# Performance work log

Measured on AMD Instinct MI355X. Metric: run time of the kernel, lower is better.

## Reference

```python
import jax, jax.numpy as jnp
import numpy as np

GAMMA = 2.0
ALPHA_CLASS = 0.01
ALPHA_COORD = 1.0

def _xywh_to_xyxy(b):
    # [.., 4] (x, y, w, h) -> (x1, y1, x2, y2)
    return jnp.concatenate([b[..., :2], b[..., :2] + b[..., 2:]], axis=-1)

def _jaccard(a, b):
    # a: [A,4] xyxy, b: [N,4] xyxy -> IoU [A,N]
    lt = jnp.maximum(a[:, None, :2], b[None, :, :2])
    rb = jnp.minimum(a[:, None, 2:], b[None, :, 2:])
    wh = jnp.clip(rb - lt, 0.0)
    inter = wh[..., 0] * wh[..., 1]
    area_a = (a[:, 2] - a[:, 0]) * (a[:, 3] - a[:, 1])
    area_b = (b[:, 2] - b[:, 0]) * (b[:, 3] - b[:, 1])
    return inter / (area_a[:, None] + area_b[None, :] - inter)

def _match_mask(thr, anchors, gt_xywh, num_obj):
    # Returns positive (anchor, gt) pair mask [A, N_max], honoring gt[:num_obj].
    A = anchors.shape[0]
    N = gt_xywh.shape[0]
    gt_boxes = _xywh_to_xyxy(gt_xywh)
    ious = _jaccard(anchors, gt_boxes)              # [A, N]
    valid = jnp.arange(N) < num_obj                 # [N]
    ious_v = jnp.where(valid[None, :], ious, -jnp.inf)
    best_gt_idx = jnp.argmax(ious_v, axis=0)        # [N] best anchor per gt
    forced = jnp.arange(A)[:, None] == best_gt_idx[None, :]  # positive_mask[best,i]=1
    return ((ious > thr) | forced) & valid[None, :]

def _class_loss_item(thr, classes, anchors, gt, num_obj):
    # classes: [A,2] probs (col0 = background, col1 = face)
    mask = _match_mask(thr, anchors, gt, num_obj)   # [A, N]
    counts = jnp.sum(mask, axis=1)                  # [A] multiplicity of each anchor in positive_idx
    is_pos = counts > 0                             # dedup, as index_fill_ does
    probs = jnp.where(is_pos, classes[:, 1], classes[:, 0])
    focal = -((1.0 - probs) ** GAMMA) * jnp.log(probs)
    # extra = focal_loss.index_select(0, positive_idx) keeps duplicates -> weight by counts
    extra = jnp.sum(counts.astype(focal.dtype) * focal)
    return jnp.sum(focal) + 10.0 * extra

def setup_inputs() -> dict:
    key = jax.random.key(0)
    B, A, N = 16, 131072, 64
    k1, k2, k3, k4, k5, k6 = jax.random.split(key, 6)
    # anchors in xyxy, valid boxes in [0,1]
    a_xy = jax.random.uniform(k1, (A, 2), jnp.float32, 0.0, 0.8)
    a_wh = jax.random.uniform(k2, (A, 2), jnp.float32, 0.05, 0.2)
    anchors = jnp.concatenate([a_xy, a_xy + a_wh], axis=-1)
    # class probabilities strictly in (0,1) for log()
    batch_classes = jax.random.uniform(k3, (B, A, 2), jnp.float32, 0.05, 0.95)
    g_xy = jax.random.uniform(k4, (B, N, 2), jnp.float32, 0.0, 0.8)
    g_wh = jax.random.uniform(k5, (B, N, 2), jnp.float32, 0.05, 0.2)
    batch_gt = jnp.concatenate([g_xy, g_wh], axis=-1)  # xywh
    batch_num_objects = jax.random.randint(k6, (B,), 1, N + 1, jnp.int32)
    return {
        "threshhold": jnp.float32(0.5),
        "batch_classes": batch_classes,
        "anchors": anchors,
        "batch_gt": batch_gt,
        "batch_num_objects": batch_num_objects,
    }

def reference(threshhold, batch_classes, anchors, batch_gt, batch_num_objects):
    R = batch_classes.shape[0]
    per_item = jax.vmap(lambda c, g, n: _class_loss_item(threshhold, c, anchors, g, n))
    class_loss = jnp.sum(per_item(batch_classes, batch_gt, batch_num_objects))
    class_loss = class_loss * ALPHA_CLASS / R
    # Faithful to the source: coord_loss is initialized to zero and never accumulated
    coord_loss = jnp.zeros((), batch_classes.dtype) * ALPHA_COORD / R
    total_loss = class_loss + coord_loss
    return (total_loss, class_loss, coord_loss)
```

## Files before the change

### kernel.cpp

```cpp
#include <hip/hip_runtime.h>

typedef unsigned long long ull;

#define NANCH    131072
#define NMAX     64
#define NBATCH   16
#define THREADS  256
#define APT      4
#define ACH      (THREADS*APT)
#define NPAIR    8
#define NB_CNT   ((NANCH/ACH)*NPAIR)
#define AC_ANCH  256
#define NCHUNK_A (NANCH/AC_ANCH)
#define BPB_A    (NCHUNK_A/4)
#define MAXB     16
#define NB_ARG   (MAXB*BPB_A)
#define GRID_MAIN (NB_CNT+NB_ARG)


__global__ __launch_bounds__(64) void k_setup(
    const int* __restrict__ nobj, ull* __restrict__ cells,
    int* __restrict__ pairs, int* __restrict__ lanepk, int* __restrict__ nbund)
{
    int tid = threadIdx.x;
    for (int i = tid; i < NBATCH*NMAX; i += 64) cells[i] = 0ull;
    for (int i = tid; i < MAXB*NMAX; i += 64) lanepk[i] = -1;
    __syncthreads();
    if (tid) return;
    int ord[NBATCH], key[NBATCH];
    for (int i = 0; i < NBATCH; ++i) { ord[i] = i; key[i] = nobj[i]; }
    for (int i = 1; i < NBATCH; ++i) {
        int k = key[i], o = ord[i], j = i-1;
        while (j >= 0 && key[j] < k) { key[j+1]=key[j]; ord[j+1]=ord[j]; --j; }
        key[j+1] = k; ord[j+1] = o;
    }
    for (int p = 0; p < NPAIR; ++p) {
        pairs[2*p]   = ord[p];
        pairs[2*p+1] = ord[NBATCH-1-p];
    }
    int rem[MAXB];
    int nb = 0;
    for (int i = 0; i < NBATCH; ++i) {
        int n = key[i], f = -1;
        for (int x = 0; x < nb; ++x) if (rem[x] >= n) { f = x; break; }
        if (f < 0) { f = nb++; rem[f] = NMAX; }
        int st = NMAX - rem[f];
        for (int k = 0; k < n; ++k) lanepk[f*NMAX + st + k] = (ord[i] << 8) | k;
        rem[f] -= n;
    }
    *nbund = nb;
}

__global__ __launch_bounds__(THREADS, 6) void k_main(
    const float* __restrict__ thr_p,
    const float* __restrict__ classes,
    const float* __restrict__ anchors,
    const float* __restrict__ gt,
    const int*   __restrict__ nobj,
    const int*   __restrict__ pairs,
    const int*   __restrict__ lanepk,
    const int*   __restrict__ nbund,
    ull* __restrict__ cells,
    double* __restrict__ partials)
{
    int bid = blockIdx.x;
    int tid = threadIdx.x;
    float thr = *thr_p;
    float q   = thr / (1.0f + thr);

    if (bid < NB_CNT) {
        int chunk = bid >> 3, pr = bid & 7;
        int b0 = pairs[2*pr], b1 = pairs[2*pr+1];
        int no0 = nobj[b0], no1 = nobj[b1];

        __shared__ float4 sbox[2*NMAX];
        __shared__ float  sqg[2*NMAX];
        __shared__ double sw[4];
        if (tid < 2*NMAX) {
            int s = tid >> 6, n = tid & 63;
            int b  = s ? b1 : b0;
            int no = s ? no1 : no0;
            float4 g = reinterpret_cast<const float4*>(gt)[b*NMAX + n];
            float x2 = g.x + g.z, y2 = g.y + g.w;
            float4 box = make_float4(g.x, g.y, x2, y2);
            float  qg  = q * ((x2 - g.x) * (y2 - g.y));
            if (n >= no) { box = make_float4(4.f,4.f,4.f,4.f); qg = __builtin_inff(); }
            sbox[tid] = box; sqg[tid] = qg;
        }
        __syncthreads();

        float ax1[APT], ay1[APT], ax2[APT], ay2[APT], qa[APT];
        int abase = chunk * ACH + tid;
        #pragma unroll
        for (int k = 0; k < APT; ++k) {
            float4 v = reinterpret_cast<const float4*>(anchors)[abase + k*THREADS];
            ax1[k]=v.x; ay1[k]=v.y; ax2[k]=v.z; ay2[k]=v.w;
            qa[k] = q * ((v.z - v.x) * (v.w - v.y));
        }

        int wv = tid >> 6, ln = tid & 63;
        double acc = 0.0;
        #pragma unroll
        for (int s = 0; s < 2; ++s) {
            int b    = s ? b1 : b0;
            int no   = s ? no1 : no0;
            int no4  = (no + 3) & ~3;
            int base = s * NMAX;
            int cnt[APT];
            #pragma unroll
            for (int k = 0; k < APT; ++k) cnt[k] = 0;

            for (int n = 0; n < no4; n += 4) {
                #pragma unroll
                for (int u = 0; u < 4; ++u) {
                    float4 g  = sbox[base + n + u];
                    float  qg = sqg[base + n + u];
                    #pragma unroll
                    for (int k = 0; k < APT; ++k) {
                        float lx = fmaxf(ax1[k], g.x);
                        float ly = fmaxf(ay1[k], g.y);
                        float rx = fminf(ax2[k], g.z);
                        float ry = fminf(ay2[k], g.w);
                        float w  = fmaxf(rx - lx, 0.f);
                        float h  = fmaxf(ry - ly, 0.f);
                        float inter = w * h;
                        cnt[k] += (inter > qa[k] + qg) ? 1 : 0;
                    }
                }
            }
            const float2* cp = reinterpret_cast<const float2*>(classes) + (size_t)b * NANCH;
            #pragma unroll
            for (int k = 0; k < APT; ++k) {
                float2 c = cp[abase + k*THREADS];
                float p  = (cnt[k] > 0) ? c.y : c.x;
                float om = 1.0f - p;
                float f  = -om * om * __logf(p);
                acc += (double)(f * (1.0f + 10.0f * (float)cnt[k]));
            }
        }
        #pragma unroll
        for (int off = 32; off; off >>= 1) acc += __shfl_xor(acc, off, 64);
        if (ln == 0) sw[wv] = acc;
        __syncthreads();
        if (tid == 0) partials[bid] = sw[0] + sw[1] + sw[2] + sw[3];

    } else {
        int r    = bid - NB_CNT;
        int bu   = r >> 7;
        int blkc = r & (BPB_A - 1);
        if (bu >= *nbund) return;
        int wv = tid >> 6, ln = tid & 63;
        int abase = (blkc*4 + wv) * AC_ANCH;

        int lp = lanepk[bu*NMAX + ln];
        bool valid = lp >= 0;
        int gidx = valid ? ((lp >> 8)*NMAX + (lp & 255)) : 0;
        float4 gg = reinterpret_cast<const float4*>(gt)[gidx];
        float gx2 = gg.x + gg.z, gy2 = gg.y + gg.w;
        float gar = (gx2 - gg.x) * (gy2 - gg.y);

        float bn[4] = {-1.f,-1.f,-1.f,-1.f};
        float bs[4] = { 1.f, 1.f, 1.f, 1.f};
        int   bj[4] = {0,0,0,0};
        const float4* ap = reinterpret_cast<const float4*>(anchors) + abase;
        for (int j = 0; j < AC_ANCH; j += 4) {
            #pragma unroll
            for (int u = 0; u < 4; ++u) {
                float4 v = ap[j + u];
                float aar = (v.z - v.x) * (v.w - v.y);
                float lx = fmaxf(v.x, gg.x);
                float ly = fmaxf(v.y, gg.y);
                float rx = fminf(v.z, gx2);
                float ry = fminf(v.w, gy2);
                float w  = fmaxf(rx - lx, 0.f);
                float h  = fmaxf(ry - ly, 0.f);
                float inter = w * h;
                float sa    = aar + gar;
                bool better = inter * bs[u] > bn[u] * sa;
                bn[u] = better ? inter : bn[u];
                bs[u] = better ? sa    : bs[u];
                bj[u] = better ? (j+u) : bj[u];
            }
        }
        if (valid) {
            ull best = 0;
            #pragma unroll
            for (int u = 0; u < 4; ++u) {
                float rr = bn[u] * __builtin_amdgcn_rcpf(bs[u]);
                unsigned aidx = (unsigned)(abase + bj[u]);
                ull pk = ((ull)__float_as_uint(rr) << 32)
                       | (ull)(0x7FFFFFFFu - aidx);
                best = pk > best ? pk : best;
            }
            atomicMax(&cells[(lp >> 8)*NMAX + (lp & 255)], best);
        }
    }
}

__global__ __launch_bounds__(1024) void k_tail(
    const float* __restrict__ thr_p,
    const float* __restrict__ classes,
    const float* __restrict__ anchors,
    const float* __restrict__ gt,
    const int*   __restrict__ nobj,
    const ull*   __restrict__ cells,
    const double* __restrict__ partials,
    float* __restrict__ out)
{
    int tid = threadIdx.x;
    int b = tid >> 6, n = tid & 63;
    float thr = *thr_p;
    float q   = thr / (1.0f + thr);

    __shared__ float4 sbox[NBATCH*NMAX];
    __shared__ float  sqg[NBATCH*NMAX];
    __shared__ int    sidx[NBATCH*NMAX];
    __shared__ double sdelta[NBATCH];
    __shared__ double sw[16];

    int n_obj = nobj[b];
    {
        float4 g = reinterpret_cast<const float4*>(gt)[b*NMAX + n];
        float x2 = g.x + g.z, y2 = g.y + g.w;
        sbox[tid] = make_float4(g.x, g.y, x2, y2);
        float gar = (x2 - g.x) * (y2 - g.y);
        sqg[tid]  = q * gar;
    }
    __syncthreads();

    int bi = -1; bool need = false;
    float4 av = make_float4(0.f,0.f,0.f,0.f);
    float qa = 0.f;
    if (n < n_obj) {
        ull pkv = cells[tid];
        bi = (int)(0x7FFFFFFFu - (unsigned)(pkv & 0xFFFFFFFFull));
        av = reinterpret_cast<const float4*>(anchors)[bi];
        float aar = (av.z - av.x) * (av.w - av.y);
        qa = q * aar;
        float4 g = sbox[tid];
        float lx = fmaxf(av.x, g.x), ly = fmaxf(av.y, g.y);
        float rx = fminf(av.z, g.z), ry = fminf(av.w, g.w);
        float w  = fmaxf(rx - lx, 0.f), h = fmaxf(ry - ly, 0.f);
        float inter = w * h;
        need = !(inter > qa + sqg[tid]);
    }
    sidx[tid] = need ? bi : -1;
    __syncthreads();

    double delta = 0.0;
    if (need) {
        bool first = true; int extra = 0;
        int base = b * NMAX;
        for (int m = 0; m < NMAX; ++m) {
            if (sidx[base + m] == bi) { if (m < n) first = false; ++extra; }
        }
        if (first) {
            int count = 0;
            for (int m = 0; m < n_obj; ++m) {
                float4 g = sbox[base + m];
                float lx = fmaxf(av.x, g.x), ly = fmaxf(av.y, g.y);
                float rx = fminf(av.z, g.z), ry = fminf(av.w, g.w);
                float w  = fmaxf(rx - lx, 0.f), h = fmaxf(ry - ly, 0.f);
                float inter = w * h;
                count += (inter > qa + sqg[base + m]) ? 1 : 0;
            }
            float2 c = reinterpret_cast<const float2*>(classes)[(size_t)b * NANCH + bi];
            float po = (count > 0) ? c.y : c.x;
            float oo = 1.0f - po;
            float fo = -oo * oo * __logf(po);
            float oldc = fo * (1.0f + 10.0f * (float)count);
            int cn = count + extra;
            float pn = (cn > 0) ? c.y : c.x;
            float on = 1.0f - pn;
            float fn = -on * on * __logf(pn);
            float newc = fn * (1.0f + 10.0f * (float)cn);
            delta = (double)newc - (double)oldc;
        }
    }
    #pragma unroll
    for (int off = 32; off; off >>= 1) delta += __shfl_xor(delta, off, 64);
    if (n == 0) sdelta[b] = delta;
    __syncthreads();

    double v = partials[tid];
    if (tid < NBATCH) v += sdelta[tid];
    #pragma unroll
    for (int off = 32; off; off >>= 1) v += __shfl_xor(v, off, 64);
    if ((tid & 63) == 0) sw[tid >> 6] = v;
    __syncthreads();
    if (tid == 0) {
        double tot = 0.0;
        #pragma unroll
        for (int i = 0; i < 16; ++i) tot += sw[i];
        double cls = tot * (0.01 / 16.0);
        out[0] = (float)cls;
        out[1] = (float)cls;
        out[2] = 0.0f;
    }
}

extern "C" void kernel_launch(void* const* d_in, const int* in_sizes, int n_in,
                              void* d_out, int out_size, void* d_ws, size_t ws_size,
                              hipStream_t stream) {
    const float* thr     = (const float*)d_in[0];
    const float* classes = (const float*)d_in[1];
    const float* anchors = (const float*)d_in[2];
    const float* gt      = (const float*)d_in[3];
    const int*   nobj    = (const int*)d_in[4];
    float* out = (float*)d_out;

    char* ws = (char*)d_ws;
    ull*    cells    = (ull*)(ws + 0);
    int*    pairs    = (int*)(ws + 8192);
    int*    lanepk   = (int*)(ws + 8256);
    int*    nbund    = (int*)(ws + 12352);
    double* partials = (double*)(ws + 12416);

    k_setup<<<1, 64, 0, stream>>>(nobj, cells, pairs, lanepk, nbund);
    k_main<<<GRID_MAIN, THREADS, 0, stream>>>(thr, classes, anchors, gt, nobj,
                                              pairs, lanepk, nbund, cells, partials);
    k_tail<<<1, 1024, 0, stream>>>(thr, classes, anchors, gt, nobj, cells, partials, out);
}
```

Before: 106.9 us.

## Precompute anchor areas, interleave count/argmax blocks, widen argmax unroll to 8

The setup kernel now precomputes the area of each anchor into the workspace when it is large enough, and the argmax path reads those areas instead of recomputing them. The argmax inner loop is unrolled 8-wide with 8 independent best-so-far accumulators and loads all eight anchors before computing. Count blocks and argmax blocks are interleaved 1:2 across the grid so the two work types run side by side instead of in two phases. The occupancy hint on k_main is dropped. The extra accumulators raise register pressure, and the setup kernel does an additional pass over the anchors.

```diff
diff --git a/kernel.cpp b/kernel.cpp
--- a/kernel.cpp
+++ b/kernel.cpp
@@ -11,20 +11,31 @@
 #define NPAIR    8
 #define NB_CNT   ((NANCH/ACH)*NPAIR)
 #define AC_ANCH  256
-#define NCHUNK_A (NANCH/AC_ANCH)
-#define BPB_A    (NCHUNK_A/4)
+#define BPB_A    128
 #define MAXB     16
 #define NB_ARG   (MAXB*BPB_A)
 #define GRID_MAIN (NB_CNT+NB_ARG)
 
-
-__global__ __launch_bounds__(64) void k_setup(
-    const int* __restrict__ nobj, ull* __restrict__ cells,
-    int* __restrict__ pairs, int* __restrict__ lanepk, int* __restrict__ nbund)
+#define WS_PAREA_OFF 24576
+#define WS_NEED (WS_PAREA_OFF + NANCH*4)
+
+template<bool BIG>
+__global__ __launch_bounds__(256) void k_setup(
+    const int* __restrict__ nobj, const float* __restrict__ anchors,
+    ull* __restrict__ cells, int* __restrict__ pairs,
+    int* __restrict__ lanepk, int* __restrict__ nbund,
+    float* __restrict__ parea)
 {
     int tid = threadIdx.x;
-    for (int i = tid; i < NBATCH*NMAX; i += 64) cells[i] = 0ull;
-    for (int i = tid; i < MAXB*NMAX; i += 64) lanepk[i] = -1;
+    if (BIG) {
+        for (int i = blockIdx.x*256 + tid; i < NANCH; i += gridDim.x*256) {
+            float4 v = reinterpret_cast<const float4*>(anchors)[i];
+            parea[i] = (v.z - v.x) * (v.w - v.y);
+        }
+    }
+    if (blockIdx.x != 0) return;
+    for (int i = tid; i < NBATCH*NMAX; i += 256) cells[i] = 0ull;
+    for (int i = tid; i < MAXB*NMAX; i += 256) lanepk[i] = -1;
     __syncthreads();
     if (tid) return;
     int ord[NBATCH], key[NBATCH];
@@ -51,7 +62,8 @@
     *nbund = nb;
 }
 
-__global__ __launch_bounds__(THREADS, 6) void k_main(
+template<bool BIG>
+__global__ __launch_bounds__(THREADS) void k_main(
     const float* __restrict__ thr_p,
     const float* __restrict__ classes,
     const float* __restrict__ anchors,
@@ -60,15 +72,18 @@
     const int*   __restrict__ pairs,
     const int*   __restrict__ lanepk,
     const int*   __restrict__ nbund,
+    const float* __restrict__ parea,
     ull* __restrict__ cells,
     double* __restrict__ partials)
 {
-    int bid = blockIdx.x;
-    int tid = threadIdx.x;
+    int bid0 = blockIdx.x;
+    int tid  = threadIdx.x;
     float thr = *thr_p;
     float q   = thr / (1.0f + thr);
-
-    if (bid < NB_CNT) {
+    bool is_cnt = (bid0 % 3) == 0;
+    int  bid    = is_cnt ? (bid0 / 3) : ((bid0 / 3) * 2 + (bid0 % 3) - 1);
+
+    if (is_cnt) {
         int chunk = bid >> 3, pr = bid & 7;
         int b0 = pairs[2*pr], b1 = pairs[2*pr+1];
         int no0 = nobj[b0], no1 = nobj[b1];
@@ -145,9 +160,8 @@
         if (tid == 0) partials[bid] = sw[0] + sw[1] + sw[2] + sw[3];
 
     } else {
-        int r    = bid - NB_CNT;
-        int bu   = r >> 7;
-        int blkc = r & (BPB_A - 1);
+        int bu   = bid >> 7;
+        int blkc = bid & (BPB_A - 1);
         if (bu >= *nbund) return;
         int wv = tid >> 6, ln = tid & 63;
         int abase = (blkc*4 + wv) * AC_ANCH;
@@ -159,23 +173,34 @@
         float gx2 = gg.x + gg.z, gy2 = gg.y + gg.w;
         float gar = (gx2 - gg.x) * (gy2 - gg.y);
 
-        float bn[4] = {-1.f,-1.f,-1.f,-1.f};
-        float bs[4] = { 1.f, 1.f, 1.f, 1.f};
-        int   bj[4] = {0,0,0,0};
-        const float4* ap = reinterpret_cast<const float4*>(anchors) + abase;
-        for (int j = 0; j < AC_ANCH; j += 4) {
-            #pragma unroll
-            for (int u = 0; u < 4; ++u) {
-                float4 v = ap[j + u];
-                float aar = (v.z - v.x) * (v.w - v.y);
-                float lx = fmaxf(v.x, gg.x);
-                float ly = fmaxf(v.y, gg.y);
-                float rx = fminf(v.z, gx2);
-                float ry = fminf(v.w, gy2);
+        float bn[8], bs[8]; int bj[8];
+        #pragma unroll
+        for (int u = 0; u < 8; ++u) { bn[u] = -1.f; bs[u] = 1.f; bj[u] = 0; }
+        const float4* ap  = reinterpret_cast<const float4*>(anchors) + abase;
+        const float4* pa4 = reinterpret_cast<const float4*>(parea + abase);
+        for (int j = 0; j < AC_ANCH; j += 8) {
+            float4 v[8]; float ar[8];
+            #pragma unroll
+            for (int u = 0; u < 8; ++u) v[u] = ap[j + u];
+            if (BIG) {
+                float4 a0 = pa4[(j >> 2)], a1 = pa4[(j >> 2) + 1];
+                ar[0]=a0.x; ar[1]=a0.y; ar[2]=a0.z; ar[3]=a0.w;
+                ar[4]=a1.x; ar[5]=a1.y; ar[6]=a1.z; ar[7]=a1.w;
+            } else {
+                #pragma unroll
+                for (int u = 0; u < 8; ++u)
+                    ar[u] = (v[u].z - v[u].x) * (v[u].w - v[u].y);
+            }
+            #pragma unroll
+            for (int u = 0; u < 8; ++u) {
+                float lx = fmaxf(v[u].x, gg.x);
+                float ly = fmaxf(v[u].y, gg.y);
+                float rx = fminf(v[u].z, gx2);
+                float ry = fminf(v[u].w, gy2);
                 float w  = fmaxf(rx - lx, 0.f);
                 float h  = fmaxf(ry - ly, 0.f);
                 float inter = w * h;
-                float sa    = aar + gar;
+                float sa    = ar[u] + gar;
                 bool better = inter * bs[u] > bn[u] * sa;
                 bn[u] = better ? inter : bn[u];
                 bs[u] = better ? sa    : bs[u];
@@ -185,7 +210,7 @@
         if (valid) {
             ull best = 0;
             #pragma unroll
-            for (int u = 0; u < 4; ++u) {
+            for (int u = 0; u < 8; ++u) {
                 float rr = bn[u] * __builtin_amdgcn_rcpf(bs[u]);
                 unsigned aidx = (unsigned)(abase + bj[u]);
                 ull pk = ((ull)__float_as_uint(rr) << 32)
@@ -315,9 +340,19 @@
     int*    lanepk   = (int*)(ws + 8256);
     int*    nbund    = (int*)(ws + 12352);
     double* partials = (double*)(ws + 12416);
-
-    k_setup<<<1, 64, 0, stream>>>(nobj, cells, pairs, lanepk, nbund);
-    k_main<<<GRID_MAIN, THREADS, 0, stream>>>(thr, classes, anchors, gt, nobj,
-                                              pairs, lanepk, nbund, cells, partials);
+    float*  parea    = (float*)(ws + WS_PAREA_OFF);
+
+    bool big = ws_size >= (size_t)WS_NEED;
+    if (big) {
+        k_setup<true><<<128, 256, 0, stream>>>(nobj, anchors, cells, pairs,
+                                               lanepk, nbund, parea);
+        k_main<true><<<GRID_MAIN, THREADS, 0, stream>>>(thr, classes, anchors, gt,
+                nobj, pairs, lanepk, nbund, parea, cells, partials);
+    } else {
+        k_setup<false><<<1, 256, 0, stream>>>(nobj, anchors, cells, pairs,
+                                              lanepk, nbund, parea);
+        k_main<false><<<GRID_MAIN, THREADS, 0, stream>>>(thr, classes, anchors, gt,
+                nobj, pairs, lanepk, nbund, parea, cells, partials);
+    }
     k_tail<<<1, 1024, 0, stream>>>(thr, classes, anchors, gt, nobj, cells, partials, out);
 }
```

Result: faster. 99.54 us (-6.9%).

## Spatially bin anchors and cull GT boxes per wave with fused argmax

Applied to the files above, without the earlier changes.

Adds a counting-sort pass (histogram, scan, scatter) that buckets anchors into a 16x16 spatial grid. The main kernel then checks each wave's anchor bounding box against each GT box and skips GT boxes that cannot overlap. The per-GT best-anchor argmax moves into the same pass, using a wave reduction plus atomicMax, so the separate full-anchor argmax sweep goes away. Background focal loss is summed over all anchors in separate blocks, and positive anchors are corrected on top. This costs three extra small launches and a larger workspace, and the old two-pass path is kept as a fallback with interleaved blocks and a wider unroll.

```diff
diff --git a/kernel.cpp b/kernel.cpp
--- a/kernel.cpp
+++ b/kernel.cpp
@@ -2,29 +2,221 @@
 
 typedef unsigned long long ull;
 
-#define NANCH    131072
-#define NMAX     64
-#define NBATCH   16
-#define THREADS  256
+#define NANCH   131072
+#define NMAX    64
+#define NBATCH  16
+#define THREADS 256
+
+#define OFF_PART  8192
+#define OFF_CH    16384
+#define OFF_CID   278528
+#define OFF_SRT   802816
+#define OFF_SIX   2899968
+#define WS_NEED   3424256
+#define OFF_PAIRS 16384
+#define OFF_LANE  16448
+#define OFF_NB    20544
+
+__device__ __forceinline__ float focal_f(float p) {
+    float om = 1.0f - p;
+    return -om * om * __logf(p);
+}
+
+__global__ __launch_bounds__(256) void k_hist(
+    const float* __restrict__ anchors, int* __restrict__ cellid,
+    int* __restrict__ chunkH)
+{
+    __shared__ int h[256];
+    int tid = threadIdx.x, c = blockIdx.x;
+    h[tid] = 0; __syncthreads();
+    #pragma unroll
+    for (int k = 0; k < 2; ++k) {
+        int i = c*512 + tid + k*256;
+        float4 v = reinterpret_cast<const float4*>(anchors)[i];
+        int cx = (int)(v.x * 20.0f); cx = cx < 0 ? 0 : (cx > 15 ? 15 : cx);
+        int cy = (int)(v.y * 20.0f); cy = cy < 0 ? 0 : (cy > 15 ? 15 : cy);
+        int cell = cy*16 + cx;
+        cellid[i] = cell;
+        atomicAdd(&h[cell], 1);
+    }
+    __syncthreads();
+    chunkH[c*256 + tid] = h[tid];
+}
+
+__global__ __launch_bounds__(256) void k_scan(
+    int* __restrict__ CH, ull* __restrict__ cells)
+{
+    __shared__ int total[256];
+    __shared__ int cstart[256];
+    int b = threadIdx.x;
+    int run = 0;
+    for (int c = 0; c < 256; ++c) { int h = CH[c*256+b]; CH[c*256+b] = run; run += h; }
+    total[b] = run;
+    __syncthreads();
+    if (b == 0) { int cs = 0; for (int i = 0; i < 256; ++i) { cstart[i] = cs; cs += total[i]; } }
+    __syncthreads();
+    int s = cstart[b];
+    for (int c = 0; c < 256; ++c) CH[c*256+b] += s;
+    for (int i = b; i < NBATCH*NMAX; i += 256) cells[i] = 0x7FFFFFFFull;
+}
+
+__global__ __launch_bounds__(256) void k_scatter(
+    const float* __restrict__ anchors, const int* __restrict__ cellid,
+    const int* __restrict__ CB, float4* __restrict__ sorted,
+    int* __restrict__ sidx)
+{
+    __shared__ int lc[512];
+    int tid = threadIdx.x, c = blockIdx.x;
+    lc[tid]     = cellid[c*512 + tid];
+    lc[tid+256] = cellid[c*512 + 256 + tid];
+    __syncthreads();
+    int i0 = 2*tid, i1 = 2*tid + 1;
+    int c0 = lc[i0], c1 = lc[i1];
+    int r0 = 0, r1 = 0;
+    for (int j = 0; j < i0; ++j) { int cj = lc[j]; r0 += (cj==c0)?1:0; r1 += (cj==c1)?1:0; }
+    r1 += (c0 == c1) ? 1 : 0;
+    int g0 = c*512 + i0, g1 = c*512 + i1;
+    int p0 = CB[c*256 + c0] + r0, p1 = CB[c*256 + c1] + r1;
+    sorted[p0] = reinterpret_cast<const float4*>(anchors)[g0]; sidx[p0] = g0;
+    sorted[p1] = reinterpret_cast<const float4*>(anchors)[g1]; sidx[p1] = g1;
+}
+
+__global__ __launch_bounds__(THREADS) void k_main_s(
+    const float* __restrict__ thr_p,
+    const float* __restrict__ classes,
+    const float4* __restrict__ sorted,
+    const int*   __restrict__ sidx,
+    const float* __restrict__ gt,
+    const int*   __restrict__ nobj,
+    ull* __restrict__ cells,
+    double* __restrict__ partials)
+{
+    int bid = blockIdx.x, tid = threadIdx.x;
+    int wv = tid >> 6, ln = tid & 63;
+    float thr = *thr_p;
+    float q   = thr / (1.0f + thr);
+    __shared__ double sw[4];
+    double acc = 0.0;
+
+    if ((bid & 1) == 0) {
+        int aid  = bid >> 1;
+        int sblk = aid >> 2, bg = aid & 3;
+        __shared__ float4 sgt[4*64];
+        __shared__ float2 sgq[4*64];
+        __shared__ int    snobj[4];
+        {
+            int bb = tid >> 6, n = tid & 63;
+            int b = bg + 4*bb;
+            float4 g = reinterpret_cast<const float4*>(gt)[b*NMAX + n];
+            float x2 = g.x + g.z, y2 = g.y + g.w;
+            sgt[tid] = make_float4(g.x, g.y, x2, y2);
+            float gar = (x2 - g.x) * (y2 - g.y);
+            sgq[tid] = make_float2(q * gar, gar);
+            if (n == 0) snobj[bb] = nobj[b];
+        }
+        __syncthreads();
+
+        int abase = sblk*1024 + wv*256;
+        float4 A[4]; float aar[4], qa[4]; int orig[4];
+        float bx1 = 1e30f, by1 = 1e30f, bx2 = -1e30f, by2 = -1e30f;
+        #pragma unroll
+        for (int k = 0; k < 4; ++k) {
+            int s = abase + k*64 + ln;
+            A[k] = sorted[s]; orig[k] = sidx[s];
+            aar[k] = (A[k].z - A[k].x) * (A[k].w - A[k].y);
+            qa[k]  = q * aar[k];
+            bx1 = fminf(bx1, A[k].x); by1 = fminf(by1, A[k].y);
+            bx2 = fmaxf(bx2, A[k].z); by2 = fmaxf(by2, A[k].w);
+        }
+        #pragma unroll
+        for (int off = 32; off; off >>= 1) {
+            bx1 = fminf(bx1, __shfl_xor(bx1, off, 64));
+            by1 = fminf(by1, __shfl_xor(by1, off, 64));
+            bx2 = fmaxf(bx2, __shfl_xor(bx2, off, 64));
+            by2 = fmaxf(by2, __shfl_xor(by2, off, 64));
+        }
+
+        const float2* cls2 = reinterpret_cast<const float2*>(classes);
+        for (int bb = 0; bb < 4; ++bb) {
+            int b = bg + 4*bb, no = snobj[bb], base = bb*64;
+            int cnt[4] = {0,0,0,0};
+            for (int n = 0; n < no; ++n) {
+                float4 g = sgt[base + n];
+                if (!(g.x < bx2 && g.z > bx1 && g.y < by2 && g.w > by1)) continue;
+                float2 gq = sgq[base + n];
+                ull mypk = 0;
+                #pragma unroll
+                for (int k = 0; k < 4; ++k) {
+                    float lx = fmaxf(A[k].x, g.x);
+                    float ly = fmaxf(A[k].y, g.y);
+                    float rx = fminf(A[k].z, g.z);
+                    float ry = fminf(A[k].w, g.w);
+                    float w  = fmaxf(rx - lx, 0.f);
+                    float h  = fmaxf(ry - ly, 0.f);
+                    float inter = w * h;
+                    cnt[k] += (inter > qa[k] + gq.x) ? 1 : 0;
+                    float sa = aar[k] + gq.y;
+                    float r  = inter * __builtin_amdgcn_rcpf(sa);
+                    ull pk = ((ull)__float_as_uint(r) << 32)
+                           | (ull)(0x7FFFFFFFu - (unsigned)orig[k]);
+                    mypk = pk > mypk ? pk : mypk;
+                }
+                #pragma unroll
+                for (int off = 32; off; off >>= 1) {
+                    ull o = __shfl_xor(mypk, off, 64);
+                    mypk = o > mypk ? o : mypk;
+                }
+                if (ln == 0) atomicMax(&cells[b*NMAX + n], mypk);
+            }
+            int any = cnt[0] | cnt[1] | cnt[2] | cnt[3];
+            if (__ballot(any != 0)) {
+                #pragma unroll
+                for (int k = 0; k < 4; ++k) {
+                    if (cnt[k] > 0) {
+                        float2 cc = cls2[(size_t)b * NANCH + orig[k]];
+                        float fg  = focal_f(cc.y);
+                        float bgf = focal_f(cc.x);
+                        acc += (double)(fg * (1.0f + 10.0f * (float)cnt[k]))
+                             - (double)bgf;
+                    }
+                }
+            }
+        }
+    } else {
+        int rid = bid >> 1;
+        const float4* c4 = reinterpret_cast<const float4*>(classes);
+        size_t base = (size_t)rid * 2048 + tid;
+        #pragma unroll
+        for (int it = 0; it < 8; ++it) {
+            float4 v = c4[base + (size_t)it * 256];
+            acc += (double)focal_f(v.x) + (double)focal_f(v.z);
+        }
+    }
+
+    #pragma unroll
+    for (int off = 32; off; off >>= 1) acc += __shfl_xor(acc, off, 64);
+    if (ln == 0) sw[wv] = acc;
+    __syncthreads();
+    if (tid == 0) partials[bid] = sw[0] + sw[1] + sw[2] + sw[3];
+}
+
 #define APT      4
 #define ACH      (THREADS*APT)
 #define NPAIR    8
 #define NB_CNT   ((NANCH/ACH)*NPAIR)
 #define AC_ANCH  256
-#define NCHUNK_A (NANCH/AC_ANCH)
-#define BPB_A    (NCHUNK_A/4)
+#define BPB_A    128
 #define MAXB     16
 #define NB_ARG   (MAXB*BPB_A)
-#define GRID_MAIN (NB_CNT+NB_ARG)
-
-
-__global__ __launch_bounds__(64) void k_setup(
+#define GRID_FB  (NB_CNT+NB_ARG)
+
+__global__ __launch_bounds__(256) void k_setup_fb(
     const int* __restrict__ nobj, ull* __restrict__ cells,
     int* __restrict__ pairs, int* __restrict__ lanepk, int* __restrict__ nbund)
 {
     int tid = threadIdx.x;
-    for (int i = tid; i < NBATCH*NMAX; i += 64) cells[i] = 0ull;
-    for (int i = tid; i < MAXB*NMAX; i += 64) lanepk[i] = -1;
+    for (int i = tid; i < NBATCH*NMAX; i += 256) cells[i] = 0ull;
+    for (int i = tid; i < MAXB*NMAX; i += 256) lanepk[i] = -1;
     __syncthreads();
     if (tid) return;
     int ord[NBATCH], key[NBATCH];
@@ -34,12 +226,8 @@
         while (j >= 0 && key[j] < k) { key[j+1]=key[j]; ord[j+1]=ord[j]; --j; }
         key[j+1] = k; ord[j+1] = o;
     }
-    for (int p = 0; p < NPAIR; ++p) {
-        pairs[2*p]   = ord[p];
-        pairs[2*p+1] = ord[NBATCH-1-p];
-    }
-    int rem[MAXB];
-    int nb = 0;
+    for (int p = 0; p < NPAIR; ++p) { pairs[2*p] = ord[p]; pairs[2*p+1] = ord[NBATCH-1-p]; }
+    int rem[MAXB]; int nb = 0;
     for (int i = 0; i < NBATCH; ++i) {
         int n = key[i], f = -1;
         for (int x = 0; x < nb; ++x) if (rem[x] >= n) { f = x; break; }
@@ -51,28 +239,23 @@
     *nbund = nb;
 }
 
-__global__ __launch_bounds__(THREADS, 6) void k_main(
-    const float* __restrict__ thr_p,
-    const float* __restrict__ classes,
-    const float* __restrict__ anchors,
-    const float* __restrict__ gt,
-    const int*   __restrict__ nobj,
-    const int*   __restrict__ pairs,
-    const int*   __restrict__ lanepk,
-    const int*   __restrict__ nbund,
-    ull* __restrict__ cells,
-    double* __restrict__ partials)
-{
-    int bid = blockIdx.x;
-    int tid = threadIdx.x;
+__global__ __launch_bounds__(THREADS) void k_main_fb(
+    const float* __restrict__ thr_p, const float* __restrict__ classes,
+    const float* __restrict__ anchors, const float* __restrict__ gt,
+    const int* __restrict__ nobj, const int* __restrict__ pairs,
+    const int* __restrict__ lanepk, const int* __restrict__ nbund,
+    ull* __restrict__ cells, double* __restrict__ partials)
+{
+    int bid0 = blockIdx.x, tid = threadIdx.x;
     float thr = *thr_p;
     float q   = thr / (1.0f + thr);
-
-    if (bid < NB_CNT) {
+    bool is_cnt = (bid0 % 3) == 0;
+    int  bid    = is_cnt ? (bid0 / 3) : ((bid0 / 3) * 2 + (bid0 % 3) - 1);
+
+    if (is_cnt) {
         int chunk = bid >> 3, pr = bid & 7;
         int b0 = pairs[2*pr], b1 = pairs[2*pr+1];
         int no0 = nobj[b0], no1 = nobj[b1];
-
         __shared__ float4 sbox[2*NMAX];
         __shared__ float  sqg[2*NMAX];
         __shared__ double sw[4];
@@ -88,7 +271,6 @@
             sbox[tid] = box; sqg[tid] = qg;
         }
         __syncthreads();
-
         float ax1[APT], ay1[APT], ax2[APT], ay2[APT], qa[APT];
         int abase = chunk * ACH + tid;
         #pragma unroll
@@ -97,32 +279,27 @@
             ax1[k]=v.x; ay1[k]=v.y; ax2[k]=v.z; ay2[k]=v.w;
             qa[k] = q * ((v.z - v.x) * (v.w - v.y));
         }
-
         int wv = tid >> 6, ln = tid & 63;
         double acc = 0.0;
         #pragma unroll
         for (int s = 0; s < 2; ++s) {
-            int b    = s ? b1 : b0;
-            int no   = s ? no1 : no0;
-            int no4  = (no + 3) & ~3;
-            int base = s * NMAX;
+            int b = s ? b1 : b0, no = s ? no1 : no0;
+            int no4 = (no + 3) & ~3, base = s * NMAX;
             int cnt[APT];
             #pragma unroll
             for (int k = 0; k < APT; ++k) cnt[k] = 0;
-
             for (int n = 0; n < no4; n += 4) {
                 #pragma unroll
                 for (int u = 0; u < 4; ++u) {
-                    float4 g  = sbox[base + n + u];
-                    float  qg = sqg[base + n + u];
+                    float4 g = sbox[base + n + u];
+                    float qg = sqg[base + n + u];
                     #pragma unroll
                     for (int k = 0; k < APT; ++k) {
                         float lx = fmaxf(ax1[k], g.x);
                         float ly = fmaxf(ay1[k], g.y);
                         float rx = fminf(ax2[k], g.z);
                         float ry = fminf(ay2[k], g.w);
-                        float w  = fmaxf(rx - lx, 0.f);
-                        float h  = fmaxf(ry - ly, 0.f);
+                        float w = fmaxf(rx - lx, 0.f), h = fmaxf(ry - ly, 0.f);
                         float inter = w * h;
                         cnt[k] += (inter > qa[k] + qg) ? 1 : 0;
                     }
@@ -132,9 +309,8 @@
             #pragma unroll
             for (int k = 0; k < APT; ++k) {
                 float2 c = cp[abase + k*THREADS];
-                float p  = (cnt[k] > 0) ? c.y : c.x;
-                float om = 1.0f - p;
-                float f  = -om * om * __logf(p);
+                float p = (cnt[k] > 0) ? c.y : c.x;
+                float f = focal_f(p);
                 acc += (double)(f * (1.0f + 10.0f * (float)cnt[k]));
             }
         }
@@ -143,39 +319,31 @@
         if (ln == 0) sw[wv] = acc;
         __syncthreads();
         if (tid == 0) partials[bid] = sw[0] + sw[1] + sw[2] + sw[3];
-
     } else {
-        int r    = bid - NB_CNT;
-        int bu   = r >> 7;
-        int blkc = r & (BPB_A - 1);
+        int bu = bid >> 7, blkc = bid & (BPB_A - 1);
         if (bu >= *nbund) return;
         int wv = tid >> 6, ln = tid & 63;
         int abase = (blkc*4 + wv) * AC_ANCH;
-
         int lp = lanepk[bu*NMAX + ln];
         bool valid = lp >= 0;
         int gidx = valid ? ((lp >> 8)*NMAX + (lp & 255)) : 0;
         float4 gg = reinterpret_cast<const float4*>(gt)[gidx];
         float gx2 = gg.x + gg.z, gy2 = gg.y + gg.w;
         float gar = (gx2 - gg.x) * (gy2 - gg.y);
-
-        float bn[4] = {-1.f,-1.f,-1.f,-1.f};
-        float bs[4] = { 1.f, 1.f, 1.f, 1.f};
-        int   bj[4] = {0,0,0,0};
+        float bn[8], bs[8]; int bj[8];
+        #pragma unroll
+        for (int u = 0; u < 8; ++u) { bn[u] = -1.f; bs[u] = 1.f; bj[u] = 0; }
         const float4* ap = reinterpret_cast<const float4*>(anchors) + abase;
-        for (int j = 0; j < AC_ANCH; j += 4) {
+        for (int j = 0; j < AC_ANCH; j += 8) {
             #pragma unroll
-            for (int u = 0; u < 4; ++u) {
+            for (int u = 0; u < 8; ++u) {
                 float4 v = ap[j + u];
                 float aar = (v.z - v.x) * (v.w - v.y);
-                float lx = fmaxf(v.x, gg.x);
-                float ly = fmaxf(v.y, gg.y);
-                float rx = fminf(v.z, gx2);
-                float ry = fminf(v.w, gy2);
-                float w  = fmaxf(rx - lx, 0.f);
-                float h  = fmaxf(ry - ly, 0.f);
+                float lx = fmaxf(v.x, gg.x), ly = fmaxf(v.y, gg.y);
+                float rx = fminf(v.z, gx2),  ry = fminf(v.w, gy2);
+                float w = fmaxf(rx - lx, 0.f), h = fmaxf(ry - ly, 0.f);
                 float inter = w * h;
-                float sa    = aar + gar;
+                float sa = aar + gar;
                 bool better = inter * bs[u] > bn[u] * sa;
                 bn[u] = better ? inter : bn[u];
                 bs[u] = better ? sa    : bs[u];
@@ -185,11 +353,10 @@
         if (valid) {
             ull best = 0;
             #pragma unroll
-            for (int u = 0; u < 4; ++u) {
+            for (int u = 0; u < 8; ++u) {
                 float rr = bn[u] * __builtin_amdgcn_rcpf(bs[u]);
                 unsigned aidx = (unsigned)(abase + bj[u]);
-                ull pk = ((ull)__float_as_uint(rr) << 32)
-                       | (ull)(0x7FFFFFFFu - aidx);
+                ull pk = ((ull)__float_as_uint(rr) << 32) | (ull)(0x7FFFFFFFu - aidx);
                 best = pk > best ? pk : best;
             }
             atomicMax(&cells[(lp >> 8)*NMAX + (lp & 255)], best);
@@ -198,14 +365,10 @@
 }
 
 __global__ __launch_bounds__(1024) void k_tail(
-    const float* __restrict__ thr_p,
-    const float* __restrict__ classes,
-    const float* __restrict__ anchors,
-    const float* __restrict__ gt,
-    const int*   __restrict__ nobj,
-    const ull*   __restrict__ cells,
-    const double* __restrict__ partials,
-    float* __restrict__ out)
+    const float* __restrict__ thr_p, const float* __restrict__ classes,
+    const float* __restrict__ anchors, const float* __restrict__ gt,
+    const int* __restrict__ nobj, const ull* __restrict__ cells,
+    const double* __restrict__ partials, float* __restrict__ out)
 {
     int tid = threadIdx.x;
     int b = tid >> 6, n = tid & 63;
@@ -214,7 +377,7 @@
 
     __shared__ float4 sbox[NBATCH*NMAX];
     __shared__ float  sqg[NBATCH*NMAX];
-    __shared__ int    sidx[NBATCH*NMAX];
+    __shared__ int    sidxs[NBATCH*NMAX];
     __shared__ double sdelta[NBATCH];
     __shared__ double sw[16];
 
@@ -240,11 +403,11 @@
         float4 g = sbox[tid];
         float lx = fmaxf(av.x, g.x), ly = fmaxf(av.y, g.y);
         float rx = fminf(av.z, g.z), ry = fminf(av.w, g.w);
-        float w  = fmaxf(rx - lx, 0.f), h = fmaxf(ry - ly, 0.f);
+        float w = fmaxf(rx - lx, 0.f), h = fmaxf(ry - ly, 0.f);
         float inter = w * h;
         need = !(inter > qa + sqg[tid]);
     }
-    sidx[tid] = need ? bi : -1;
+    sidxs[tid] = need ? bi : -1;
     __syncthreads();
 
     double delta = 0.0;
@@ -252,7 +415,7 @@
         bool first = true; int extra = 0;
         int base = b * NMAX;
         for (int m = 0; m < NMAX; ++m) {
-            if (sidx[base + m] == bi) { if (m < n) first = false; ++extra; }
+            if (sidxs[base + m] == bi) { if (m < n) first = false; ++extra; }
         }
         if (first) {
             int count = 0;
@@ -260,19 +423,17 @@
                 float4 g = sbox[base + m];
                 float lx = fmaxf(av.x, g.x), ly = fmaxf(av.y, g.y);
                 float rx = fminf(av.z, g.z), ry = fminf(av.w, g.w);
-                float w  = fmaxf(rx - lx, 0.f), h = fmaxf(ry - ly, 0.f);
+                float w = fmaxf(rx - lx, 0.f), h = fmaxf(ry - ly, 0.f);
                 float inter = w * h;
                 count += (inter > qa + sqg[base + m]) ? 1 : 0;
             }
             float2 c = reinterpret_cast<const float2*>(classes)[(size_t)b * NANCH + bi];
             float po = (count > 0) ? c.y : c.x;
-            float oo = 1.0f - po;
-            float fo = -oo * oo * __logf(po);
+            float fo = focal_f(po);
             float oldc = fo * (1.0f + 10.0f * (float)count);
             int cn = count + extra;
             float pn = (cn > 0) ? c.y : c.x;
-            float on = 1.0f - pn;
-            float fn = -on * on * __logf(pn);
+            float fn = focal_f(pn);
             float newc = fn * (1.0f + 10.0f * (float)cn);
             delta = (double)newc - (double)oldc;
         }
@@ -311,13 +472,25 @@
 
     char* ws = (char*)d_ws;
     ull*    cells    = (ull*)(ws + 0);
-    int*    pairs    = (int*)(ws + 8192);
-    int*    lanepk   = (int*)(ws + 8256);
-    int*    nbund    = (int*)(ws + 12352);
-    double* partials = (double*)(ws + 12416);
-
-    k_setup<<<1, 64, 0, stream>>>(nobj, cells, pairs, lanepk, nbund);
-    k_main<<<GRID_MAIN, THREADS, 0, stream>>>(thr, classes, anchors, gt, nobj,
-                                              pairs, lanepk, nbund, cells, partials);
+    double* partials = (double*)(ws + OFF_PART);
+
+    if (ws_size >= (size_t)WS_NEED) {
+        int*    CH     = (int*)(ws + OFF_CH);
+        int*    cellid = (int*)(ws + OFF_CID);
+        float4* sorted = (float4*)(ws + OFF_SRT);
+        int*    sidx   = (int*)(ws + OFF_SIX);
+        k_hist<<<256, 256, 0, stream>>>(anchors, cellid, CH);
+        k_scan<<<1, 256, 0, stream>>>(CH, cells);
+        k_scatter<<<256, 256, 0, stream>>>(anchors, cellid, CH, sorted, sidx);
+        k_main_s<<<1024, THREADS, 0, stream>>>(thr, classes, sorted, sidx,
+                                               gt, nobj, cells, partials);
+    } else {
+        int* pairs  = (int*)(ws + OFF_PAIRS);
+        int* lanepk = (int*)(ws + OFF_LANE);
+        int* nbund  = (int*)(ws + OFF_NB);
+        k_setup_fb<<<1, 256, 0, stream>>>(nobj, cells, pairs, lanepk, nbund);
+        k_main_fb<<<GRID_FB, THREADS, 0, stream>>>(thr, classes, anchors, gt, nobj,
+                                                   pairs, lanepk, nbund, cells, partials);
+    }
     k_tail<<<1, 1024, 0, stream>>>(thr, classes, anchors, gt, nobj, cells, partials, out);
 }
```

Result: slower. 133.1 us (+24.5%).

## Interleave count/argmax blocks, double-buffer anchor loads, parallelize lanepk fill

Applied to the files above, without the earlier changes.

Block indices are interleaved so that every third block runs the counting path and the other two run the argmax path. This spreads the two workloads evenly across CUs instead of running all counting blocks first. The argmax loop now keeps 8 independent running maxima and software-prefetches the next 8 anchors into registers, giving more ILP and hiding load latency. The launch_bounds occupancy hint is dropped, and the lanepk fill in setup is spread across threads. The risks are higher register pressure and lower occupancy.

```diff
diff --git a/kernel.cpp b/kernel.cpp
--- a/kernel.cpp
+++ b/kernel.cpp
@@ -11,12 +11,16 @@
 #define NPAIR    8
 #define NB_CNT   ((NANCH/ACH)*NPAIR)
 #define AC_ANCH  256
-#define NCHUNK_A (NANCH/AC_ANCH)
-#define BPB_A    (NCHUNK_A/4)
+#define BPB_A    128
 #define MAXB     16
 #define NB_ARG   (MAXB*BPB_A)
 #define GRID_MAIN (NB_CNT+NB_ARG)
 
+
+__device__ __forceinline__ float focal_f(float p) {
+    float om = 1.0f - p;
+    return -om * om * __logf(p);
+}
 
 __global__ __launch_bounds__(64) void k_setup(
     const int* __restrict__ nobj, ull* __restrict__ cells,
@@ -25,33 +29,39 @@
     int tid = threadIdx.x;
     for (int i = tid; i < NBATCH*NMAX; i += 64) cells[i] = 0ull;
     for (int i = tid; i < MAXB*NMAX; i += 64) lanepk[i] = -1;
-    __syncthreads();
-    if (tid) return;
-    int ord[NBATCH], key[NBATCH];
-    for (int i = 0; i < NBATCH; ++i) { ord[i] = i; key[i] = nobj[i]; }
-    for (int i = 1; i < NBATCH; ++i) {
-        int k = key[i], o = ord[i], j = i-1;
-        while (j >= 0 && key[j] < k) { key[j+1]=key[j]; ord[j+1]=ord[j]; --j; }
-        key[j+1] = k; ord[j+1] = o;
-    }
-    for (int p = 0; p < NPAIR; ++p) {
-        pairs[2*p]   = ord[p];
-        pairs[2*p+1] = ord[NBATCH-1-p];
-    }
-    int rem[MAXB];
-    int nb = 0;
+
+    __shared__ int s_b[NBATCH], s_no[NBATCH], s_bu[NBATCH], s_st[NBATCH];
+    if (tid == 0) {
+        int ord[NBATCH], key[NBATCH];
+        for (int i = 0; i < NBATCH; ++i) { ord[i] = i; key[i] = nobj[i]; }
+        for (int i = 1; i < NBATCH; ++i) {
+            int k = key[i], o = ord[i], j = i-1;
+            while (j >= 0 && key[j] < k) { key[j+1]=key[j]; ord[j+1]=ord[j]; --j; }
+            key[j+1] = k; ord[j+1] = o;
+        }
+        for (int p = 0; p < NPAIR; ++p) {
+            pairs[2*p]   = ord[p];
+            pairs[2*p+1] = ord[NBATCH-1-p];
+        }
+        int rem[MAXB]; int nb = 0;
+        for (int i = 0; i < NBATCH; ++i) {
+            int n = key[i], f = -1;
+            for (int x = 0; x < nb; ++x) if (rem[x] >= n) { f = x; break; }
+            if (f < 0) { f = nb++; rem[f] = NMAX; }
+            s_b[i] = ord[i]; s_no[i] = n; s_bu[i] = f; s_st[i] = NMAX - rem[f];
+            rem[f] -= n;
+        }
+        *nbund = nb;
+    }
+    __syncthreads();
+    #pragma unroll
     for (int i = 0; i < NBATCH; ++i) {
-        int n = key[i], f = -1;
-        for (int x = 0; x < nb; ++x) if (rem[x] >= n) { f = x; break; }
-        if (f < 0) { f = nb++; rem[f] = NMAX; }
-        int st = NMAX - rem[f];
-        for (int k = 0; k < n; ++k) lanepk[f*NMAX + st + k] = (ord[i] << 8) | k;
-        rem[f] -= n;
-    }
-    *nbund = nb;
-}
-
-__global__ __launch_bounds__(THREADS, 6) void k_main(
+        if (tid < s_no[i])
+            lanepk[s_bu[i]*NMAX + s_st[i] + tid] = (s_b[i] << 8) | tid;
+    }
+}
+
+__global__ __launch_bounds__(THREADS) void k_main(
     const float* __restrict__ thr_p,
     const float* __restrict__ classes,
     const float* __restrict__ anchors,
@@ -63,12 +73,14 @@
     ull* __restrict__ cells,
     double* __restrict__ partials)
 {
-    int bid = blockIdx.x;
-    int tid = threadIdx.x;
+    int bid0 = blockIdx.x;
+    int tid  = threadIdx.x;
     float thr = *thr_p;
     float q   = thr / (1.0f + thr);
-
-    if (bid < NB_CNT) {
+    bool is_cnt = (bid0 % 3) == 0;
+    int  bid    = is_cnt ? (bid0 / 3) : ((bid0 / 3) * 2 + (bid0 % 3) - 1);
+
+    if (is_cnt) {
         int chunk = bid >> 3, pr = bid & 7;
         int b0 = pairs[2*pr], b1 = pairs[2*pr+1];
         int no0 = nobj[b0], no1 = nobj[b1];
@@ -133,8 +145,7 @@
             for (int k = 0; k < APT; ++k) {
                 float2 c = cp[abase + k*THREADS];
                 float p  = (cnt[k] > 0) ? c.y : c.x;
-                float om = 1.0f - p;
-                float f  = -om * om * __logf(p);
+                float f  = focal_f(p);
                 acc += (double)(f * (1.0f + 10.0f * (float)cnt[k]));
             }
         }
@@ -145,9 +156,8 @@
         if (tid == 0) partials[bid] = sw[0] + sw[1] + sw[2] + sw[3];
 
     } else {
-        int r    = bid - NB_CNT;
-        int bu   = r >> 7;
-        int blkc = r & (BPB_A - 1);
+        int bu   = bid >> 7;
+        int blkc = bid & (BPB_A - 1);
         if (bu >= *nbund) return;
         int wv = tid >> 6, ln = tid & 63;
         int abase = (blkc*4 + wv) * AC_ANCH;
@@ -159,21 +169,25 @@
         float gx2 = gg.x + gg.z, gy2 = gg.y + gg.w;
         float gar = (gx2 - gg.x) * (gy2 - gg.y);
 
-        float bn[4] = {-1.f,-1.f,-1.f,-1.f};
-        float bs[4] = { 1.f, 1.f, 1.f, 1.f};
-        int   bj[4] = {0,0,0,0};
+        float bn[8], bs[8]; int bj[8];
+        #pragma unroll
+        for (int u = 0; u < 8; ++u) { bn[u] = -1.f; bs[u] = 1.f; bj[u] = 0; }
         const float4* ap = reinterpret_cast<const float4*>(anchors) + abase;
-        for (int j = 0; j < AC_ANCH; j += 4) {
+
+        float4 va[4], vb[4];
+        #pragma unroll
+        for (int u = 0; u < 4; ++u) va[u] = ap[u];
+        #pragma unroll
+        for (int u = 0; u < 4; ++u) vb[u] = ap[4 + u];
+        for (int j = 0; j < AC_ANCH; j += 8) {
+            int jn = (j + 8 < AC_ANCH) ? (j + 8) : j;
             #pragma unroll
             for (int u = 0; u < 4; ++u) {
-                float4 v = ap[j + u];
+                float4 v = va[u];
                 float aar = (v.z - v.x) * (v.w - v.y);
-                float lx = fmaxf(v.x, gg.x);
-                float ly = fmaxf(v.y, gg.y);
-                float rx = fminf(v.z, gx2);
-                float ry = fminf(v.w, gy2);
-                float w  = fmaxf(rx - lx, 0.f);
-                float h  = fmaxf(ry - ly, 0.f);
+                float lx = fmaxf(v.x, gg.x), ly = fmaxf(v.y, gg.y);
+                float rx = fminf(v.z, gx2),  ry = fminf(v.w, gy2);
+                float w  = fmaxf(rx - lx, 0.f), h = fmaxf(ry - ly, 0.f);
                 float inter = w * h;
                 float sa    = aar + gar;
                 bool better = inter * bs[u] > bn[u] * sa;
@@ -181,11 +195,30 @@
                 bs[u] = better ? sa    : bs[u];
                 bj[u] = better ? (j+u) : bj[u];
             }
+            #pragma unroll
+            for (int u = 0; u < 4; ++u) va[u] = ap[jn + u];
+            #pragma unroll
+            for (int u = 0; u < 4; ++u) {
+                float4 v = vb[u];
+                float aar = (v.z - v.x) * (v.w - v.y);
+                float lx = fmaxf(v.x, gg.x), ly = fmaxf(v.y, gg.y);
+                float rx = fminf(v.z, gx2),  ry = fminf(v.w, gy2);
+                float w  = fmaxf(rx - lx, 0.f), h = fmaxf(ry - ly, 0.f);
+                float inter = w * h;
+                float sa    = aar + gar;
+                int c = 4 + u;
+                bool better = inter * bs[c] > bn[c] * sa;
+                bn[c] = better ? inter     : bn[c];
+                bs[c] = better ? sa        : bs[c];
+                bj[c] = better ? (j+4+u)   : bj[c];
+            }
+            #pragma unroll
+            for (int u = 0; u < 4; ++u) vb[u] = ap[jn + 4 + u];
         }
         if (valid) {
             ull best = 0;
             #pragma unroll
-            for (int u = 0; u < 4; ++u) {
+            for (int u = 0; u < 8; ++u) {
                 float rr = bn[u] * __builtin_amdgcn_rcpf(bs[u]);
                 unsigned aidx = (unsigned)(abase + bj[u]);
                 ull pk = ((ull)__float_as_uint(rr) << 32)
@@ -266,13 +299,11 @@
             }
             float2 c = reinterpret_cast<const float2*>(classes)[(size_t)b * NANCH + bi];
             float po = (count > 0) ? c.y : c.x;
-            float oo = 1.0f - po;
-            float fo = -oo * oo * __logf(po);
+            float fo = focal_f(po);
             float oldc = fo * (1.0f + 10.0f * (float)count);
             int cn = count + extra;
             float pn = (cn > 0) ? c.y : c.x;
-            float on = 1.0f - pn;
-            float fn = -on * on * __logf(pn);
+            float fn = focal_f(pn);
             float newc = fn * (1.0f + 10.0f * (float)cn);
             delta = (double)newc - (double)oldc;
         }
```

New measurement: 95.53 us. -10.7%, faster.
